# Performance work log

Hardware: AMD Instinct MI355X
Metric: run time of the kernel (lower is better)

Reference implementation:

```python
import jax, jax.numpy as jnp
import numpy as np

H = 2048          # hidden_size
NQ = 16           # num_q_heads
NKV = 4           # num_kv_heads
HD = H // NQ      # head_dim = 128
REP = NQ // NKV   # kv repeat factor
FF = 8192         # intermediate_size
B, S = 2, 2048
EPS = 1e-6


def setup_inputs() -> dict:
    key = jax.random.key(0)
    ks = jax.random.split(key, 12)
    sd = 0.02
    return {
        "hidden_states": jax.random.normal(ks[0], (B, S, H), jnp.float32),
        "Wq": jax.random.normal(ks[1], (H, H), jnp.float32) * sd,
        "bq": jnp.zeros((H,), jnp.float32),
        "Wk": jax.random.normal(ks[2], (H, NKV * HD), jnp.float32) * sd,
        "bk": jnp.zeros((NKV * HD,), jnp.float32),
        "Wv": jax.random.normal(ks[3], (H, NKV * HD), jnp.float32) * sd,
        "bv": jnp.zeros((NKV * HD,), jnp.float32),
        "Wo": jax.random.normal(ks[4], (H, H), jnp.float32) * sd,
        "bo": jnp.zeros((H,), jnp.float32),
        "W1": jax.random.normal(ks[5], (H, FF), jnp.float32) * sd,
        "b1": jnp.zeros((FF,), jnp.float32),
        "W2": jax.random.normal(ks[6], (FF, H), jnp.float32) * sd,
        "b2": jnp.zeros((H,), jnp.float32),
        "g1": jnp.ones((H,), jnp.float32),  # ln1 weight
        "g2": jnp.ones((H,), jnp.float32),  # ln2 weight
    }


def _rmsnorm(x, g):
    rms = jnp.sqrt(jnp.mean(x * x, axis=-1, keepdims=True) + EPS)
    return g * (x / rms)


def _attention(x, Wq, bq, Wk, bk, Wv, bv, Wo, bo):
    b, s, _ = x.shape
    q = (x @ Wq + bq).reshape(b, s, NQ, HD).transpose(0, 2, 1, 3)    # [b,hq,s,d]
    k = (x @ Wk + bk).reshape(b, s, NKV, HD).transpose(0, 2, 1, 3)   # [b,hkv,s,d]
    v = (x @ Wv + bv).reshape(b, s, NKV, HD).transpose(0, 2, 1, 3)
    k = jnp.repeat(k, REP, axis=1)  # GQA: repeat_interleave over head dim
    v = jnp.repeat(v, REP, axis=1)
    scale = 1.0 / np.sqrt(HD).astype(np.float32)
    scores = jnp.einsum("bhqd,bhkd->bhqk", q, k) * scale
    causal = jnp.triu(jnp.ones((s, s), bool), k=1)                   # True above diag
    scores = jnp.where(causal[None, None], -jnp.inf, scores)
    probs = jax.nn.softmax(scores, axis=-1)
    ctx = jnp.einsum("bhqk,bhkd->bhqd", probs, v)
    ctx = ctx.transpose(0, 2, 1, 3).reshape(b, s, H)
    return ctx @ Wo + bo


def reference(hidden_states, Wq, bq, Wk, bk, Wv, bv, Wo, bo, W1, b1, W2, b2, g1, g2):
    x = hidden_states
    # pre-norm attention block
    x = x + _attention(_rmsnorm(x, g1), Wq, bq, Wk, bk, Wv, bv, Wo, bo)
    # pre-norm FFN block (exact GELU, matching torch nn.GELU default)
    h = _rmsnorm(x, g2)
    h = jax.nn.gelu(h @ W1 + b1, approximate=False) @ W2 + b2
    return x + h
```

## Files before the change

kernel.cpp:

```cpp
#include <hip/hip_runtime.h>
#include <cstdint>

#define H_    2048
#define NQ_   16
#define NKV_  4
#define HD_   128
#define FF_   8192
#define B_    2
#define S_    2048
#define TOK   (B_*S_)
#define QKVN  (H_ + 2*NKV_*HD_)
#define KVB   64

typedef __bf16 bf16;
typedef bf16  bf16x8 __attribute__((ext_vector_type(8)));
typedef float f32x4  __attribute__((ext_vector_type(4)));

typedef __attribute__((address_space(1))) void as1_void;
typedef __attribute__((address_space(3))) void as3_void;

__device__ __forceinline__ void gload_lds16(const void* g, void* l) {
    __builtin_amdgcn_global_load_lds((as1_void*)g, (as3_void*)l, 16, 0, 0);
}

__global__ __launch_bounds__(256) void wtrans_kernel(
    const float* __restrict__ W, bf16* __restrict__ Wt, int K, int N, int outOff)
{
    __shared__ float tile[32][33];
    const int n0 = (int)blockIdx.x * 32;
    const int k0 = (int)blockIdx.y * 32;
    const int c  = (int)threadIdx.x & 31;
    const int r  = (int)threadIdx.x >> 5;
#pragma unroll
    for (int i = 0; i < 4; ++i)
        tile[r + i*8][c] = W[(size_t)(k0 + r + i*8) * N + n0 + c];
    __syncthreads();
#pragma unroll
    for (int i = 0; i < 4; ++i)
        Wt[(size_t)(outOff + n0 + r + i*8) * K + k0 + c] = (bf16)tile[c][r + i*8];
}

__global__ void biaspack_kernel(const float* __restrict__ bq, const float* __restrict__ bk,
                                const float* __restrict__ bv, float* __restrict__ out)
{
    const int i = (int)(blockIdx.x * 256 + threadIdx.x);
    out[i] = (i < H_) ? bq[i] : (i < H_ + NKV_*HD_ ? bk[i - H_] : bv[i - H_ - NKV_*HD_]);
}

__global__ __launch_bounds__(256) void rmsnorm_kernel(
    const float* __restrict__ x, const float* __restrict__ g, bf16* __restrict__ y)
{
    const int row = (int)blockIdx.x;
    const int tid = (int)threadIdx.x;
    const float* xr = x + (size_t)row * H_;
    const float4 a = *(const float4*)(xr + tid*8);
    const float4 c = *(const float4*)(xr + tid*8 + 4);
    float ss = a.x*a.x + a.y*a.y + a.z*a.z + a.w*a.w
             + c.x*c.x + c.y*c.y + c.z*c.z + c.w*c.w;
#pragma unroll
    for (int d = 1; d < 64; d <<= 1) ss += __shfl_xor(ss, d);
    __shared__ float red[4];
    if ((tid & 63) == 0) red[tid >> 6] = ss;
    __syncthreads();
    const float inv = rsqrtf((red[0]+red[1]+red[2]+red[3]) * (1.0f/H_) + 1e-6f);
    const float vals[8] = {a.x,a.y,a.z,a.w,c.x,c.y,c.z,c.w};
    const float* gp = g + tid*8;
    bf16x8 outv;
#pragma unroll
    for (int e = 0; e < 8; ++e) outv[e] = (bf16)(vals[e] * inv * gp[e]);
    *(bf16x8*)(y + (size_t)row * H_ + tid*8) = outv;
}

__global__ __launch_bounds__(256) void vtrans_kernel(
    const bf16* __restrict__ qkv, bf16* __restrict__ Vt)
{
    __shared__ bf16 tile[32][33];
    const int tt = (int)blockIdx.x;
    const int d0 = (int)blockIdx.y * 32;
    const int kh = (int)blockIdx.z;
    const int b  = (tt*32) / S_;
    const int s0 = (tt*32) % S_;
    const int c = (int)threadIdx.x & 31;
    const int r = (int)threadIdx.x >> 5;
#pragma unroll
    for (int i = 0; i < 4; ++i)
        tile[r + i*8][c] = qkv[(size_t)(tt*32 + r + i*8)*QKVN + H_ + NKV_*HD_ + kh*HD_ + d0 + c];
    __syncthreads();
#pragma unroll
    for (int i = 0; i < 4; ++i)
        Vt[((size_t)(b*NKV_ + kh)*HD_ + d0 + r + i*8)*S_ + s0 + c] = tile[c][r + i*8];
}

template<int MODE>
__global__ __launch_bounds__(512, 2) void gemm3_kernel(
    const bf16* __restrict__ A, const bf16* __restrict__ Bt,
    const float* __restrict__ bias, const float* __restrict__ resid,
    void* __restrict__ Cout, int M, int N, int Kf, int Ks)
{
    __shared__ bf16 lA[2][256*64];
    __shared__ bf16 lB[2][256*64];
    const int tid  = (int)threadIdx.x;
    const int wid  = tid >> 6;
    const int lane = tid & 63;
    const int lr   = lane & 15;
    const int lg   = lane >> 4;
    const int z    = (int)blockIdx.z;
    const int kOff = z * Ks;

    const int gx  = (int)gridDim.x;
    const int nwg = gx * (int)gridDim.y;
    int wg = (int)blockIdx.y * gx + (int)blockIdx.x;
    wg = (wg & 7) * (nwg >> 3) + (wg >> 3);
    const int nsup  = gx >> 2;
    const int chunk = wg >> 5;
    const int cin   = wg & 31;
    const int m0 = ((chunk / nsup) * 8 + (cin >> 2)) * 256;
    const int n0 = ((chunk % nsup) * 4 + (cin & 3)) * 256;

    const int wm = wid >> 2;
    const int wn = wid & 3;

    const int r8    = lane >> 3;
    const int octA  = (lane & 7) ^ (((lane >> 5) & 1) << 1);
    const int octB  = octA ^ 4;
    const bf16* aB0 = A  + (size_t)(m0 + wid*16 + r8) * Kf + kOff + octA*8;
    const bf16* aB1 = A  + (size_t)(m0 + wid*16 + 8 + r8) * Kf + kOff + octB*8;
    const bf16* bB0 = Bt + (size_t)(n0 + wid*16 + r8) * Kf + kOff + octA*8;
    const bf16* bB1 = Bt + (size_t)(n0 + wid*16 + 8 + r8) * Kf + kOff + octB*8;

    const int NT = Ks / 64;
    const int NITER = NT / 2;

    auto stA = [&](int k, int half, int buf) {
        const size_t ka = (size_t)k * 64;
        gload_lds16(aB0 + (size_t)half*128*Kf + ka, &lA[buf][(half*128 + wid*16    )*64]);
        gload_lds16(aB1 + (size_t)half*128*Kf + ka, &lA[buf][(half*128 + wid*16 + 8)*64]);
    };
    auto stB = [&](int k, int half, int buf) {
        const size_t ka = (size_t)k * 64;
        gload_lds16(bB0 + (size_t)half*128*Kf + ka, &lB[buf][(half*128 + wid*16    )*64]);
        gload_lds16(bB1 + (size_t)half*128*Kf + ka, &lB[buf][(half*128 + wid*16 + 8)*64]);
    };
    auto rd = [&](const bf16* base, int row, int kk) -> bf16x8 {
        const int swz = (((row >> 2) & 1) << 4) | (((row >> 3) & 1) << 5);
        return *(const bf16x8*)&base[row*64 + ((kk*32 + lg*8) ^ swz)];
    };

    f32x4 acc[8][4] = {};
    bf16x8 fa[4][2], fb0[2][2], fb1[2][2];

    stA(0,0,0); stB(0,0,0); stB(0,1,0); stA(0,1,0);
    stA(1,0,1); stB(1,0,1); stB(1,1,1);
    asm volatile("s_waitcnt vmcnt(6)" ::: "memory");
    __builtin_amdgcn_s_barrier();

#define MFMA_CLUSTER(ACCR, FB)                                              \
    __builtin_amdgcn_s_setprio(1);                                          \
    _Pragma("unroll") for (int kk = 0; kk < 2; ++kk)                        \
    _Pragma("unroll") for (int mf = 0; mf < 4; ++mf)                        \
    _Pragma("unroll") for (int nf = 0; nf < 2; ++nf)                        \
        acc[ACCR][(FB) ? nf+2 : nf] = __builtin_amdgcn_mfma_f32_16x16x32_bf16( \
            fa[mf][kk], ((FB) ? fb1 : fb0)[nf][kk], acc[ACCR][(FB) ? nf+2 : nf], 0, 0, 0); \
    __builtin_amdgcn_s_setprio(0);                                          \
    __builtin_amdgcn_sched_barrier(0);

    for (int t = 0; t < NITER; ++t) {
        const int kb0 = 2*t, kb1 = 2*t + 1;
        const bool s2 = (kb0 + 2) < NT;
        const bool s3 = (kb1 + 2) < NT;
        const bool lastGate = (t == NITER - 1);

#pragma unroll
        for (int mf = 0; mf < 4; ++mf) { fa[mf][0] = rd(lA[0], wm*64 + mf*16 + lr, 0);
                                         fa[mf][1] = rd(lA[0], wm*64 + mf*16 + lr, 1); }
#pragma unroll
        for (int nf = 0; nf < 2; ++nf) { fb0[nf][0] = rd(lB[0], wn*64 + nf*16 + lr, 0);
                                         fb0[nf][1] = rd(lB[0], wn*64 + nf*16 + lr, 1); }
        stA(kb1, 1, 1);
        __builtin_amdgcn_s_barrier();
        asm volatile("s_waitcnt lgkmcnt(0)" ::: "memory");
        __builtin_amdgcn_sched_barrier(0);
        MFMA_CLUSTER(mf, 0)
        __builtin_amdgcn_s_barrier();

#pragma unroll
        for (int nf = 0; nf < 2; ++nf) { fb1[nf][0] = rd(lB[0], wn*64 + 32 + nf*16 + lr, 0);
                                         fb1[nf][1] = rd(lB[0], wn*64 + 32 + nf*16 + lr, 1); }
        if (s2) stA(kb0 + 2, 0, 0);
        __builtin_amdgcn_s_barrier();
        asm volatile("s_waitcnt lgkmcnt(0)" ::: "memory");
        __builtin_amdgcn_sched_barrier(0);
        MFMA_CLUSTER(mf, 1)
        __builtin_amdgcn_s_barrier();

#pragma unroll
        for (int mf = 0; mf < 4; ++mf) { fa[mf][0] = rd(lA[0], 128 + wm*64 + mf*16 + lr, 0);
                                         fa[mf][1] = rd(lA[0], 128 + wm*64 + mf*16 + lr, 1); }
        if (s2) stB(kb0 + 2, 0, 0);
        __builtin_amdgcn_s_barrier();
        asm volatile("s_waitcnt lgkmcnt(0)" ::: "memory");
        __builtin_amdgcn_sched_barrier(0);
        MFMA_CLUSTER(mf+4, 1)
        __builtin_amdgcn_s_barrier();

        if (s2) stB(kb0 + 2, 1, 0);
        __builtin_amdgcn_s_barrier();
        __builtin_amdgcn_sched_barrier(0);
        MFMA_CLUSTER(mf+4, 0)
        if (lastGate) { asm volatile("s_waitcnt vmcnt(0)" ::: "memory"); }
        else          { asm volatile("s_waitcnt vmcnt(6)" ::: "memory"); }
        __builtin_amdgcn_s_barrier();

#pragma unroll
        for (int mf = 0; mf < 4; ++mf) { fa[mf][0] = rd(lA[1], wm*64 + mf*16 + lr, 0);
                                         fa[mf][1] = rd(lA[1], wm*64 + mf*16 + lr, 1); }
#pragma unroll
        for (int nf = 0; nf < 2; ++nf) { fb0[nf][0] = rd(lB[1], wn*64 + nf*16 + lr, 0);
                                         fb0[nf][1] = rd(lB[1], wn*64 + nf*16 + lr, 1); }
        if (s2) stA(kb0 + 2, 1, 0);
        __builtin_amdgcn_s_barrier();
        asm volatile("s_waitcnt lgkmcnt(0)" ::: "memory");
        __builtin_amdgcn_sched_barrier(0);
        MFMA_CLUSTER(mf, 0)
        __builtin_amdgcn_s_barrier();

#pragma unroll
        for (int nf = 0; nf < 2; ++nf) { fb1[nf][0] = rd(lB[1], wn*64 + 32 + nf*16 + lr, 0);
                                         fb1[nf][1] = rd(lB[1], wn*64 + 32 + nf*16 + lr, 1); }
        if (s3) stA(kb1 + 2, 0, 1);
        __builtin_amdgcn_s_barrier();
        asm volatile("s_waitcnt lgkmcnt(0)" ::: "memory");
        __builtin_amdgcn_sched_barrier(0);
        MFMA_CLUSTER(mf, 1)
        __builtin_amdgcn_s_barrier();

#pragma unroll
        for (int mf = 0; mf < 4; ++mf) { fa[mf][0] = rd(lA[1], 128 + wm*64 + mf*16 + lr, 0);
                                         fa[mf][1] = rd(lA[1], 128 + wm*64 + mf*16 + lr, 1); }
        if (s3) stB(kb1 + 2, 0, 1);
        __builtin_amdgcn_s_barrier();
        asm volatile("s_waitcnt lgkmcnt(0)" ::: "memory");
        __builtin_amdgcn_sched_barrier(0);
        MFMA_CLUSTER(mf+4, 1)
        __builtin_amdgcn_s_barrier();

        if (s3) stB(kb1 + 2, 1, 1);
        __builtin_amdgcn_s_barrier();
        __builtin_amdgcn_sched_barrier(0);
        MFMA_CLUSTER(mf+4, 0)
        if (!lastGate) { asm volatile("s_waitcnt vmcnt(6)" ::: "memory"); }
        __builtin_amdgcn_s_barrier();
    }
#undef MFMA_CLUSTER

#pragma unroll
    for (int nf = 0; nf < 4; ++nf) {
        const int col = n0 + wn*64 + nf*16 + lr;
        const float bj = (MODE == 3) ? 0.f : bias[col];
#pragma unroll
        for (int mf = 0; mf < 8; ++mf) {
            const int row0 = m0 + (mf >> 2)*128 + wm*64 + (mf & 3)*16 + lg*4;
#pragma unroll
            for (int rr = 0; rr < 4; ++rr) {
                float v = acc[mf][nf][rr] + bj;
                const size_t idx = (size_t)(row0 + rr) * N + col;
                if (MODE == 2) {
                    ((float*)Cout)[idx] = v + resid[idx];
                } else if (MODE == 3) {
                    ((bf16*)Cout)[(size_t)z * M * N + idx] = (bf16)v;
                } else {
                    if (MODE == 1) v = 0.5f * v * (1.0f + erff(v * 0.70710678118654752f));
                    ((bf16*)Cout)[idx] = (bf16)v;
                }
            }
        }
    }
}

__global__ __launch_bounds__(256) void reduce2_kernel(
    const bf16* __restrict__ part, const float* __restrict__ bias,
    const float* __restrict__ resid, float* __restrict__ out)
{
    const size_t i0 = ((size_t)blockIdx.x * 256 + threadIdx.x) * 8;
    const bf16x8 p0 = *(const bf16x8*)(part + i0);
    const bf16x8 p1 = *(const bf16x8*)(part + (size_t)TOK*H_ + i0);
    const int col = (int)(i0 & (H_ - 1));
    const float4 r0 = *(const float4*)(resid + i0);
    const float4 r1 = *(const float4*)(resid + i0 + 4);
    const float4 b0 = *(const float4*)(bias + col);
    const float4 b1 = *(const float4*)(bias + col + 4);
    float4 o0, o1;
    o0.x = (float)p0[0] + (float)p1[0] + b0.x + r0.x;
    o0.y = (float)p0[1] + (float)p1[1] + b0.y + r0.y;
    o0.z = (float)p0[2] + (float)p1[2] + b0.z + r0.z;
    o0.w = (float)p0[3] + (float)p1[3] + b0.w + r0.w;
    o1.x = (float)p0[4] + (float)p1[4] + b1.x + r1.x;
    o1.y = (float)p0[5] + (float)p1[5] + b1.y + r1.y;
    o1.z = (float)p0[6] + (float)p1[6] + b1.z + r1.z;
    o1.w = (float)p0[7] + (float)p1[7] + b1.w + r1.w;
    *(float4*)(out + i0)     = o0;
    *(float4*)(out + i0 + 4) = o1;
}

__global__ __launch_bounds__(256) void attn_kernel(
    const bf16* __restrict__ qkv, const bf16* __restrict__ Vt,
    bf16* __restrict__ ctx)
{
    __shared__ bf16 lK[2][KVB*HD_];
    __shared__ bf16 lV[2][HD_*KVB];
    __shared__ bf16 lP[4][16*72];
    const int tid  = (int)threadIdx.x;
    const int wid  = tid >> 6;
    const int lane = tid & 63;
    const int lr   = lane & 15;
    const int lg   = lane >> 4;
    const int qt = (int)gridDim.x - 1 - (int)blockIdx.x;
    const int h = (int)blockIdx.y, b = (int)blockIdx.z;
    const int kh = h >> 2;
    const int qb = qt * 64;
    const int qw = qb + wid * 16;
    const float scale = 0.08838834764831845f;

    const bf16* kB[4];
    const bf16* vB[4];
#pragma unroll
    for (int i = 0; i < 4; ++i) {
        const int kRow = (wid*4 + i)*4 + (lane >> 4);
        const int kCol = ((lane & 15) ^ (kRow & 7)) * 8;
        kB[i] = qkv + (size_t)(b*S_ + kRow)*QKVN + H_ + kh*HD_ + kCol;
        const int vRow = (wid*4 + i)*8 + (lane >> 3);
        const int vCol = ((lane & 7) ^ (vRow & 7)) * 8;
        vB[i] = Vt + ((size_t)(b*NKV_ + kh)*HD_ + vRow)*S_ + vCol;
    }

    bf16x8 qf[4];
    {
        const bf16* qp = qkv + (size_t)(b*S_ + qw + lr)*QKVN + h*HD_ + lg*8;
#pragma unroll
        for (int t = 0; t < 4; ++t) qf[t] = *(const bf16x8*)(qp + t*32);
    }

    f32x4 o[8] = {};
    float mrow[4] = {-__builtin_inff(), -__builtin_inff(), -__builtin_inff(), -__builtin_inff()};
    float lrow[4] = {0.f, 0.f, 0.f, 0.f};
    const int nt = qt + 1;

#pragma unroll
    for (int i = 0; i < 4; ++i) {
        gload_lds16(kB[i], &lK[0][(wid*4 + i)*4*HD_]);
        gload_lds16(vB[i], &lV[0][(wid*4 + i)*8*KVB]);
    }

    int cur = 0;
    for (int t = 0; t < nt; ++t) {
        __syncthreads();
        if (t + 1 < nt) {
            const size_t kAdd = (size_t)(t+1)*KVB*QKVN;
            const size_t vAdd = (size_t)(t+1)*KVB;
#pragma unroll
            for (int i = 0; i < 4; ++i) {
                gload_lds16(kB[i] + kAdd, &lK[cur^1][(wid*4 + i)*4*HD_]);
                gload_lds16(vB[i] + vAdd, &lV[cur^1][(wid*4 + i)*8*KVB]);
            }
        }
        const int kv0 = t * KVB;

        f32x4 s[4] = {};
#pragma unroll
        for (int sub = 0; sub < 4; ++sub) {
            const int krow = sub*16 + lr;
            const bf16* kr = &lK[cur][krow*HD_];
            const int swk = (krow & 7) * 8;
#pragma unroll
            for (int d = 0; d < 4; ++d) {
                const bf16x8 kf = *(const bf16x8*)(kr + ((d*32 + lg*8) ^ swk));
                s[sub] = __builtin_amdgcn_mfma_f32_16x16x32_bf16(qf[d], kf, s[sub], 0, 0, 0);
            }
        }

        float p[4][4], rmax[4];
        if (t == qt) {
#pragma unroll
            for (int rr = 0; rr < 4; ++rr) {
                const int q = qw + lg*4 + rr;
                rmax[rr] = -__builtin_inff();
#pragma unroll
                for (int sub = 0; sub < 4; ++sub) {
                    const int kv = kv0 + sub*16 + lr;
                    const float v = s[sub][rr] * scale;
                    p[sub][rr] = (kv <= q) ? v : -__builtin_inff();
                    rmax[rr] = fmaxf(rmax[rr], p[sub][rr]);
                }
            }
        } else {
#pragma unroll
            for (int rr = 0; rr < 4; ++rr) {
                rmax[rr] = -__builtin_inff();
#pragma unroll
                for (int sub = 0; sub < 4; ++sub) {
                    p[sub][rr] = s[sub][rr] * scale;
                    rmax[rr] = fmaxf(rmax[rr], p[sub][rr]);
                }
            }
        }
#pragma unroll
        for (int d = 1; d < 16; d <<= 1)
#pragma unroll
            for (int rr = 0; rr < 4; ++rr)
                rmax[rr] = fmaxf(rmax[rr], __shfl_xor(rmax[rr], d));

        float fsc[4], rsum[4];
#pragma unroll
        for (int rr = 0; rr < 4; ++rr) {
            const float mn = fmaxf(mrow[rr], rmax[rr]);
            fsc[rr]  = __expf(mrow[rr] - mn);
            mrow[rr] = mn;
            rsum[rr] = 0.f;
#pragma unroll
            for (int sub = 0; sub < 4; ++sub) {
                p[sub][rr] = __expf(p[sub][rr] - mn);
                rsum[rr] += p[sub][rr];
            }
        }
#pragma unroll
        for (int d = 1; d < 16; d <<= 1)
#pragma unroll
            for (int rr = 0; rr < 4; ++rr)
                rsum[rr] += __shfl_xor(rsum[rr], d);
#pragma unroll
        for (int rr = 0; rr < 4; ++rr) lrow[rr] = lrow[rr]*fsc[rr] + rsum[rr];
#pragma unroll
        for (int dch = 0; dch < 8; ++dch)
#pragma unroll
            for (int rr = 0; rr < 4; ++rr) o[dch][rr] *= fsc[rr];

#pragma unroll
        for (int sub = 0; sub < 4; ++sub)
#pragma unroll
            for (int rr = 0; rr < 4; ++rr)
                lP[wid][(lg*4 + rr)*72 + sub*16 + lr] = (bf16)p[sub][rr];
        bf16x8 pfr[2];
#pragma unroll
        for (int kk = 0; kk < 2; ++kk)
            pfr[kk] = *(const bf16x8*)&lP[wid][lr*72 + kk*32 + lg*8];

#pragma unroll
        for (int dch = 0; dch < 8; ++dch) {
            const bf16* vr = &lV[cur][(dch*16 + lr)*KVB];
            const int swv = (lr & 7) * 8;
#pragma unroll
            for (int kk = 0; kk < 2; ++kk) {
                const bf16x8 vf = *(const bf16x8*)(vr + ((kk*32 + lg*8) ^ swv));
                o[dch] = __builtin_amdgcn_mfma_f32_16x16x32_bf16(pfr[kk], vf, o[dch], 0, 0, 0);
            }
        }
        cur ^= 1;
    }

#pragma unroll
    for (int rr = 0; rr < 4; ++rr) {
        const float inv = 1.0f / lrow[rr];
        bf16* cp = ctx + (size_t)(b*S_ + qw + lg*4 + rr) * H_ + h*HD_ + lr;
#pragma unroll
        for (int dch = 0; dch < 8; ++dch)
            cp[dch*16] = (bf16)(o[dch][rr] * inv);
    }
}

extern "C" void kernel_launch(void* const* d_in, const int* in_sizes, int n_in,
                              void* d_out, int out_size, void* d_ws, size_t ws_size,
                              hipStream_t stream)
{
    const float* hidden = (const float*)d_in[0];
    const float* Wq = (const float*)d_in[1];
    const float* bq = (const float*)d_in[2];
    const float* Wk = (const float*)d_in[3];
    const float* bk = (const float*)d_in[4];
    const float* Wv = (const float*)d_in[5];
    const float* bv = (const float*)d_in[6];
    const float* Wo = (const float*)d_in[7];
    const float* bo = (const float*)d_in[8];
    const float* W1 = (const float*)d_in[9];
    const float* b1 = (const float*)d_in[10];
    const float* W2 = (const float*)d_in[11];
    const float* b2 = (const float*)d_in[12];
    const float* g1 = (const float*)d_in[13];
    const float* g2 = (const float*)d_in[14];
    float* out = (float*)d_out;

    char* p = (char*)d_ws;
    auto alloc = [&](size_t bytes) { char* r = p; p += (bytes + 255) & ~(size_t)255; return r; };
    bf16*  wt_qkv = (bf16*)alloc((size_t)QKVN * H_ * 2);
    bf16*  wo_t   = (bf16*)alloc((size_t)H_ * H_ * 2);
    bf16*  w1_t   = (bf16*)alloc((size_t)FF_ * H_ * 2);
    bf16*  w2_t   = (bf16*)alloc((size_t)H_ * FF_ * 2);
    float* bqkv   = (float*)alloc((size_t)QKVN * 4);
    bf16*  xn1    = (bf16*)alloc((size_t)TOK * H_ * 2);
    bf16*  qkv    = (bf16*)alloc((size_t)TOK * QKVN * 2);
    bf16*  ctxb   = (bf16*)alloc((size_t)TOK * H_ * 2);
    float* x1     = (float*)alloc((size_t)TOK * H_ * 4);
    bf16*  xn2    = (bf16*)alloc((size_t)TOK * H_ * 2);
    bf16*  ffn    = (bf16*)alloc((size_t)TOK * FF_ * 2);
    bf16*  vt     = xn1;
    bf16*  fpart  = w1_t;

    const dim3 blk(256);
    const dim3 blk3(512);
    biaspack_kernel<<<dim3(QKVN/256), blk, 0, stream>>>(bq, bk, bv, bqkv);
    wtrans_kernel<<<dim3(H_/32,  H_/32),  blk, 0, stream>>>(Wq, wt_qkv, H_, H_,  0);
    wtrans_kernel<<<dim3(512/32, H_/32),  blk, 0, stream>>>(Wk, wt_qkv, H_, 512, H_);
    wtrans_kernel<<<dim3(512/32, H_/32),  blk, 0, stream>>>(Wv, wt_qkv, H_, 512, H_ + 512);
    wtrans_kernel<<<dim3(H_/32,  H_/32),  blk, 0, stream>>>(Wo, wo_t,   H_, H_,  0);
    wtrans_kernel<<<dim3(FF_/32, H_/32),  blk, 0, stream>>>(W1, w1_t,   H_, FF_, 0);
    wtrans_kernel<<<dim3(H_/32,  FF_/32), blk, 0, stream>>>(W2, w2_t,   FF_, H_, 0);

    rmsnorm_kernel<<<dim3(TOK), blk, 0, stream>>>(hidden, g1, xn1);
    gemm3_kernel<0><<<dim3(QKVN/256, TOK/256), blk3, 0, stream>>>(
        xn1, wt_qkv, bqkv, nullptr, qkv, TOK, QKVN, H_, H_);
    vtrans_kernel<<<dim3(TOK/32, HD_/32, NKV_), blk, 0, stream>>>(qkv, vt);
    attn_kernel<<<dim3(S_/64, NQ_, B_), blk, 0, stream>>>(qkv, vt, ctxb);
    gemm3_kernel<2><<<dim3(H_/256, TOK/256), blk3, 0, stream>>>(
        ctxb, wo_t, bo, hidden, x1, TOK, H_, H_, H_);
    rmsnorm_kernel<<<dim3(TOK), blk, 0, stream>>>(x1, g2, xn2);
    gemm3_kernel<1><<<dim3(FF_/256, TOK/256), blk3, 0, stream>>>(
        xn2, w1_t, b1, nullptr, ffn, TOK, FF_, H_, H_);
    gemm3_kernel<3><<<dim3(H_/256, TOK/256, 2), blk3, 0, stream>>>(
        ffn, w2_t, nullptr, nullptr, fpart, TOK, H_, FF_, FF_/2);
    reduce2_kernel<<<dim3(TOK*H_/(256*8)), blk, 0, stream>>>(fpart, b2, x1, out);
}
```

Measured before the change: 760.4 us.

## Remap GEMM warps to 4x2 grid with 64x128 per-warp tiles and reschedule

Changes the warp layout of the 256x256 GEMM tile from 2x4 (each warp computing two 64x64 halves) to 4x2 (each warp computing one 64x128 tile). A-fragments are loaded once per k-block and reused across four B quarters, and B fragments are double-buffered so LDS reads overlap the MFMA phases, with partial lgkmcnt waits. The global-to-LDS prefetch order and vmcnt gating are also reorganised. This aims to reduce LDS read traffic per MFMA, at the cost of more complex synchronisation and a changed accumulator layout in the epilogue.

Result: no change. 760.9 us (+0.1%).

```diff
diff --git a/kernel.cpp b/kernel.cpp
--- a/kernel.cpp
+++ b/kernel.cpp
@@ -117,8 +117,8 @@
     const int m0 = ((chunk / nsup) * 8 + (cin >> 2)) * 256;
     const int n0 = ((chunk % nsup) * 4 + (cin & 3)) * 256;
 
-    const int wm = wid >> 2;
-    const int wn = wid & 3;
+    const int wm = wid >> 1;
+    const int wn = wid & 1;
 
     const int r8    = lane >> 3;
     const int octA  = (lane & 7) ^ (((lane >> 5) & 1) << 1);
@@ -146,123 +146,106 @@
         return *(const bf16x8*)&base[row*64 + ((kk*32 + lg*8) ^ swz)];
     };
 
-    f32x4 acc[8][4] = {};
-    bf16x8 fa[4][2], fb0[2][2], fb1[2][2];
-
-    stA(0,0,0); stB(0,0,0); stB(0,1,0); stA(0,1,0);
-    stA(1,0,1); stB(1,0,1); stB(1,1,1);
-    asm volatile("s_waitcnt vmcnt(6)" ::: "memory");
-    __builtin_amdgcn_s_barrier();
-
-#define MFMA_CLUSTER(ACCR, FB)                                              \
-    __builtin_amdgcn_s_setprio(1);                                          \
-    _Pragma("unroll") for (int kk = 0; kk < 2; ++kk)                        \
-    _Pragma("unroll") for (int mf = 0; mf < 4; ++mf)                        \
-    _Pragma("unroll") for (int nf = 0; nf < 2; ++nf)                        \
-        acc[ACCR][(FB) ? nf+2 : nf] = __builtin_amdgcn_mfma_f32_16x16x32_bf16( \
-            fa[mf][kk], ((FB) ? fb1 : fb0)[nf][kk], acc[ACCR][(FB) ? nf+2 : nf], 0, 0, 0); \
-    __builtin_amdgcn_s_setprio(0);                                          \
-    __builtin_amdgcn_sched_barrier(0);
+    f32x4 acc[4][8] = {};
+    bf16x8 fa[4][2];
+    bf16x8 bq[2][2][2];
+
+#define SFENCE __builtin_amdgcn_sched_barrier(0)
+#define BAR    __builtin_amdgcn_s_barrier()
+#define RD_A(BASE) _Pragma("unroll") for (int mf = 0; mf < 4; ++mf) { \
+        fa[mf][0] = rd(BASE, wm*64 + mf*16 + lr, 0);                   \
+        fa[mf][1] = rd(BASE, wm*64 + mf*16 + lr, 1); }
+#define RD_B(BASE, Q, S) _Pragma("unroll") for (int nf = 0; nf < 2; ++nf) { \
+        bq[S][nf][0] = rd(BASE, wn*128 + (Q)*32 + nf*16 + lr, 0);            \
+        bq[S][nf][1] = rd(BASE, wn*128 + (Q)*32 + nf*16 + lr, 1); }
+#define MFMA_PH(Q, S)                                                        \
+    __builtin_amdgcn_s_setprio(1);                                           \
+    _Pragma("unroll") for (int kk = 0; kk < 2; ++kk)                         \
+    _Pragma("unroll") for (int mf = 0; mf < 4; ++mf)                         \
+    _Pragma("unroll") for (int nf = 0; nf < 2; ++nf)                         \
+        acc[mf][2*(Q)+nf] = __builtin_amdgcn_mfma_f32_16x16x32_bf16(         \
+            fa[mf][kk], bq[S][nf][kk], acc[mf][2*(Q)+nf], 0, 0, 0);          \
+    __builtin_amdgcn_s_setprio(0);                                           \
+    SFENCE;
+
+    stA(0,0,0); stA(0,1,0); stB(0,0,0); stB(0,1,0);
+    stA(1,0,1);
+    asm volatile("s_waitcnt vmcnt(2)" ::: "memory");
+    BAR;
 
     for (int t = 0; t < NITER; ++t) {
         const int kb0 = 2*t, kb1 = 2*t + 1;
         const bool s2 = (kb0 + 2) < NT;
         const bool s3 = (kb1 + 2) < NT;
-        const bool lastGate = (t == NITER - 1);
-
-#pragma unroll
-        for (int mf = 0; mf < 4; ++mf) { fa[mf][0] = rd(lA[0], wm*64 + mf*16 + lr, 0);
-                                         fa[mf][1] = rd(lA[0], wm*64 + mf*16 + lr, 1); }
-#pragma unroll
-        for (int nf = 0; nf < 2; ++nf) { fb0[nf][0] = rd(lB[0], wn*64 + nf*16 + lr, 0);
-                                         fb0[nf][1] = rd(lB[0], wn*64 + nf*16 + lr, 1); }
-        stA(kb1, 1, 1);
-        __builtin_amdgcn_s_barrier();
+
+        RD_A(lA[0]); RD_B(lA  == lA ? lB[0] : lB[0], 0, 0); SFENCE;
+        RD_B(lB[0], 1, 1);
+        stB(kb1, 0, 1); stB(kb1, 1, 1); stA(kb1, 1, 1);
+        SFENCE; BAR;
+        asm volatile("s_waitcnt lgkmcnt(4)" ::: "memory"); SFENCE;
+        MFMA_PH(0, 0)
+        BAR;
+        RD_B(lB[0], 2, 0);
+        if (s2) stA(kb0 + 2, 0, 0);
+        SFENCE; BAR;
+        asm volatile("s_waitcnt lgkmcnt(4)" ::: "memory"); SFENCE;
+        MFMA_PH(1, 1)
+        BAR;
+        RD_B(lB[0], 3, 1);
+        SFENCE; BAR;
+        asm volatile("s_waitcnt lgkmcnt(4)" ::: "memory"); SFENCE;
+        MFMA_PH(2, 0)
+        BAR;
+        BAR;
         asm volatile("s_waitcnt lgkmcnt(0)" ::: "memory");
-        __builtin_amdgcn_sched_barrier(0);
-        MFMA_CLUSTER(mf, 0)
-        __builtin_amdgcn_s_barrier();
-
-#pragma unroll
-        for (int nf = 0; nf < 2; ++nf) { fb1[nf][0] = rd(lB[0], wn*64 + 32 + nf*16 + lr, 0);
-                                         fb1[nf][1] = rd(lB[0], wn*64 + 32 + nf*16 + lr, 1); }
-        if (s2) stA(kb0 + 2, 0, 0);
-        __builtin_amdgcn_s_barrier();
+        if (s2) { asm volatile("s_waitcnt vmcnt(2)" ::: "memory"); }
+        else    { asm volatile("s_waitcnt vmcnt(0)" ::: "memory"); }
+        SFENCE;
+        MFMA_PH(3, 1)
+        BAR;
+
+        RD_A(lA[1]); RD_B(lB[1], 0, 0); SFENCE;
+        RD_B(lB[1], 1, 1);
+        if (s2) { stB(kb0 + 2, 0, 0); stB(kb0 + 2, 1, 0); stA(kb0 + 2, 1, 0); }
+        SFENCE; BAR;
+        asm volatile("s_waitcnt lgkmcnt(4)" ::: "memory"); SFENCE;
+        MFMA_PH(0, 0)
+        BAR;
+        RD_B(lB[1], 2, 0);
+        if (s3) stA(kb1 + 2, 0, 1);
+        SFENCE; BAR;
+        asm volatile("s_waitcnt lgkmcnt(4)" ::: "memory"); SFENCE;
+        MFMA_PH(1, 1)
+        BAR;
+        RD_B(lB[1], 3, 1);
+        SFENCE; BAR;
+        asm volatile("s_waitcnt lgkmcnt(4)" ::: "memory"); SFENCE;
+        MFMA_PH(2, 0)
+        BAR;
+        BAR;
         asm volatile("s_waitcnt lgkmcnt(0)" ::: "memory");
-        __builtin_amdgcn_sched_barrier(0);
-        MFMA_CLUSTER(mf, 1)
-        __builtin_amdgcn_s_barrier();
-
-#pragma unroll
-        for (int mf = 0; mf < 4; ++mf) { fa[mf][0] = rd(lA[0], 128 + wm*64 + mf*16 + lr, 0);
-                                         fa[mf][1] = rd(lA[0], 128 + wm*64 + mf*16 + lr, 1); }
-        if (s2) stB(kb0 + 2, 0, 0);
-        __builtin_amdgcn_s_barrier();
-        asm volatile("s_waitcnt lgkmcnt(0)" ::: "memory");
-        __builtin_amdgcn_sched_barrier(0);
-        MFMA_CLUSTER(mf+4, 1)
-        __builtin_amdgcn_s_barrier();
-
-        if (s2) stB(kb0 + 2, 1, 0);
-        __builtin_amdgcn_s_barrier();
-        __builtin_amdgcn_sched_barrier(0);
-        MFMA_CLUSTER(mf+4, 0)
-        if (lastGate) { asm volatile("s_waitcnt vmcnt(0)" ::: "memory"); }
-        else          { asm volatile("s_waitcnt vmcnt(6)" ::: "memory"); }
-        __builtin_amdgcn_s_barrier();
-
-#pragma unroll
-        for (int mf = 0; mf < 4; ++mf) { fa[mf][0] = rd(lA[1], wm*64 + mf*16 + lr, 0);
-                                         fa[mf][1] = rd(lA[1], wm*64 + mf*16 + lr, 1); }
-#pragma unroll
-        for (int nf = 0; nf < 2; ++nf) { fb0[nf][0] = rd(lB[1], wn*64 + nf*16 + lr, 0);
-                                         fb0[nf][1] = rd(lB[1], wn*64 + nf*16 + lr, 1); }
-        if (s2) stA(kb0 + 2, 1, 0);
-        __builtin_amdgcn_s_barrier();
-        asm volatile("s_waitcnt lgkmcnt(0)" ::: "memory");
-        __builtin_amdgcn_sched_barrier(0);
-        MFMA_CLUSTER(mf, 0)
-        __builtin_amdgcn_s_barrier();
-
-#pragma unroll
-        for (int nf = 0; nf < 2; ++nf) { fb1[nf][0] = rd(lB[1], wn*64 + 32 + nf*16 + lr, 0);
-                                         fb1[nf][1] = rd(lB[1], wn*64 + 32 + nf*16 + lr, 1); }
-        if (s3) stA(kb1 + 2, 0, 1);
-        __builtin_amdgcn_s_barrier();
-        asm volatile("s_waitcnt lgkmcnt(0)" ::: "memory");
-        __builtin_amdgcn_sched_barrier(0);
-        MFMA_CLUSTER(mf, 1)
-        __builtin_amdgcn_s_barrier();
-
-#pragma unroll
-        for (int mf = 0; mf < 4; ++mf) { fa[mf][0] = rd(lA[1], 128 + wm*64 + mf*16 + lr, 0);
-                                         fa[mf][1] = rd(lA[1], 128 + wm*64 + mf*16 + lr, 1); }
-        if (s3) stB(kb1 + 2, 0, 1);
-        __builtin_amdgcn_s_barrier();
-        asm volatile("s_waitcnt lgkmcnt(0)" ::: "memory");
-        __builtin_amdgcn_sched_barrier(0);
-        MFMA_CLUSTER(mf+4, 1)
-        __builtin_amdgcn_s_barrier();
-
-        if (s3) stB(kb1 + 2, 1, 1);
-        __builtin_amdgcn_s_barrier();
-        __builtin_amdgcn_sched_barrier(0);
-        MFMA_CLUSTER(mf+4, 0)
-        if (!lastGate) { asm volatile("s_waitcnt vmcnt(6)" ::: "memory"); }
-        __builtin_amdgcn_s_barrier();
-    }
-#undef MFMA_CLUSTER
-
-#pragma unroll
-    for (int nf = 0; nf < 4; ++nf) {
-        const int col = n0 + wn*64 + nf*16 + lr;
+        if (s3) { asm volatile("s_waitcnt vmcnt(2)" ::: "memory"); }
+        else    { asm volatile("s_waitcnt vmcnt(0)" ::: "memory"); }
+        SFENCE;
+        MFMA_PH(3, 1)
+        BAR;
+    }
+#undef MFMA_PH
+#undef RD_B
+#undef RD_A
+#undef BAR
+#undef SFENCE
+
+#pragma unroll
+    for (int j = 0; j < 8; ++j) {
+        const int col = n0 + wn*128 + (j >> 1)*32 + (j & 1)*16 + lr;
         const float bj = (MODE == 3) ? 0.f : bias[col];
 #pragma unroll
-        for (int mf = 0; mf < 8; ++mf) {
-            const int row0 = m0 + (mf >> 2)*128 + wm*64 + (mf & 3)*16 + lg*4;
+        for (int mf = 0; mf < 4; ++mf) {
+            const int row0 = m0 + wm*64 + mf*16 + lg*4;
 #pragma unroll
             for (int rr = 0; rr < 4; ++rr) {
-                float v = acc[mf][nf][rr] + bj;
+                float v = acc[mf][j][rr] + bj;
                 const size_t idx = (size_t)(row0 + rr) * N + col;
                 if (MODE == 2) {
                     ((float*)Cout)[idx] = v + resid[idx];
```
